# Performance work log

Measured on AMD Instinct MI355X. Metric: run time of the kernel, lower is better.

Reference implementation:

```python
import jax, jax.numpy as jnp
import numpy as np

B, S, H = 32, 2048, 1024

def setup_inputs() -> dict:
    key = jax.random.key(0)
    ks = jax.random.split(key, 8)
    sc = 1.0 / np.sqrt(H)
    return {
        "decoder_hidden": jax.random.normal(ks[0], (B, H), jnp.float32),
        "encoder_outputs": jax.random.normal(ks[1], (B, S, H), jnp.float32),
        "mask": jax.random.randint(ks[2], (B, S), 0, 2, jnp.int32),
        "Wa_w": jax.random.normal(ks[3], (H, H), jnp.float32) * sc,
        "Wa_b": jax.random.normal(ks[4], (H,), jnp.float32) * sc,
        "Ua_w": jax.random.normal(ks[5], (H, H), jnp.float32) * sc,
        "Ua_b": jax.random.normal(ks[6], (H,), jnp.float32) * sc,
        "Va_w": jax.random.normal(ks[7], (H,), jnp.float32) * sc,
        "Va_b": jnp.float32(0.0),
    }

def reference(decoder_hidden, encoder_outputs, mask, Wa_w, Wa_b, Ua_w, Ua_b, Va_w, Va_b):
    # dec proj: [B,H] -> [B,1,H]; enc proj: [B,S,H]
    dec_proj = (decoder_hidden @ Wa_w + Wa_b)[:, None, :]
    enc_proj = jnp.einsum('bsh,hk->bsk', encoder_outputs, Ua_w) + Ua_b
    energy = jnp.tanh(dec_proj + enc_proj)                      # [B,S,H]
    scores = jnp.einsum('bsh,h->bs', energy, Va_w) + Va_b       # [B,S]
    scores = jnp.where(mask == 0, jnp.float32(-1e9), scores)
    return jax.nn.softmax(scores, axis=1)
```

## Files before the change

### kernel.cpp

```cpp
#include <hip/hip_runtime.h>
#include <math.h>

#define BB 32
#define SS 2048
#define HH 1024
#define MT (BB*SS)

#define BM 256
#define BN 256
#define BK 32
#define NT (HH/BK)
#define NCH (HH/BN)
#define THREADS 512
#define BTILE 16384

typedef float  f32x4 __attribute__((ext_vector_type(4)));
typedef short  s16x8 __attribute__((ext_vector_type(8)));
typedef unsigned short u16;

__device__ inline void split1(float x, u16& h, u16& l) {
    unsigned u = __float_as_uint(x);
    h = (u16)(u >> 16);
    float hf = __uint_as_float((u >> 16) << 16);
    l = (u16)(__float_as_uint(x - hf) >> 16);
}
__device__ inline void split8v(float4 v0, float4 v1, s16x8& h, s16x8& l) {
    float x[8] = {v0.x,v0.y,v0.z,v0.w,v1.x,v1.y,v1.z,v1.w};
    #pragma unroll
    for (int j = 0; j < 8; ++j) {
        u16 hh, ll; split1(x[j], hh, ll);
        h[j] = (short)hh; l[j] = (short)ll;
    }
}

__global__ void dec_proj_kernel(const float* __restrict__ dh,
                                const float* __restrict__ Wa_w,
                                const float* __restrict__ Wa_b,
                                const float* __restrict__ Ua_b,
                                float* __restrict__ dec_proj) {
    __shared__ float sdh[HH];
    const int b   = blockIdx.x;
    const int nq  = blockIdx.y;
    const int tid = threadIdx.x;
    for (int i = tid; i < HH; i += 256) sdh[i] = dh[b*HH + i];
    __syncthreads();
    const int n = nq*256 + tid;
    float acc = Wa_b[n] + Ua_b[n];
    for (int k = 0; k < HH; ++k)
        acc = fmaf(sdh[k], Wa_w[(size_t)k*HH + n], acc);
    dec_proj[b*HH + n] = acc;
}

__global__ void transpose_convert_kernel(const float* __restrict__ Ua,
                                         u16* __restrict__ B_pre) {
    __shared__ u16 shh[64][72], shl[64][72];
    const int nb = blockIdx.x * 64, kb = blockIdx.y * 64;
    const int tid = threadIdx.x;
    const int kl = tid >> 4, nl4 = (tid & 15) * 4;
    #pragma unroll
    for (int q = 0; q < 4; ++q) {
        const int k = kl + q*16;
        float4 v = *(const float4*)&Ua[(size_t)(kb + k)*HH + nb + nl4];
        float x[4] = {v.x, v.y, v.z, v.w};
        #pragma unroll
        for (int j = 0; j < 4; ++j) {
            u16 hh, ll; split1(x[j], hh, ll);
            shh[k][nl4 + j] = hh; shl[k][nl4 + j] = ll;
        }
    }
    __syncthreads();
    const int nl = tid >> 3, kc8 = (tid & 7) * 8;
    #pragma unroll
    for (int q = 0; q < 2; ++q) {
        const int n = nb + nl + q*32;
        const int kglob = kb + kc8;
        s16x8 hv, lv;
        #pragma unroll
        for (int j = 0; j < 8; ++j) {
            hv[j] = (short)shh[kc8 + j][nl + q*32];
            lv[j] = (short)shl[kc8 + j][nl + q*32];
        }
        const int nchI = n >> 8, fI = (n >> 4) & 15, lrI = n & 15;
        const int ktI = kglob >> 5, cI = (kglob >> 3) & 3;
        const size_t base = (size_t)(nchI*32 + ktI) * BTILE;
        const size_t idxH = base + fI*512 + (cI*16 + lrI)*8;
        *(s16x8*)&B_pre[idxH]        = hv;
        *(s16x8*)&B_pre[idxH + 8192] = lv;
    }
}

__global__ __launch_bounds__(THREADS, 1)
void gemm8_kernel(const float* __restrict__ A,
                  const u16* __restrict__ B_pre,
                  const float* __restrict__ dec_proj,
                  const float* __restrict__ Va_w,
                  float* __restrict__ partials)
{
    __shared__ __align__(16) u16 AhS[2][BM*BK];
    __shared__ __align__(16) u16 AlS[2][BM*BK];
    __shared__ __align__(16) u16 BhS[2][BN*BK];
    __shared__ __align__(16) u16 BlS[2][BN*BK];

    const int bid = blockIdx.x;
    const int wg  = (bid & 7) * 128 + (bid >> 3);
    const int nch = wg & 3;
    const int mt  = wg >> 2;
    const int m0  = mt * BM, n0 = nch * BN;

    const int tid = threadIdx.x, lane = tid & 63, wid = tid >> 6;
    const int wm = wid >> 2, wn = wid & 3;
    const int lr = lane & 15, lk = lane >> 4;

    const int srow = tid >> 1, shalf = tid & 1;
    const float* Ab = A + (size_t)(m0 + srow)*HH + shalf*16;
    const int awoff0 = (srow>>4)*512 + (shalf*2    )*128 + (srow&15)*8;
    const int awoff1 = (srow>>4)*512 + (shalf*2 + 1)*128 + (srow&15)*8;
    const u16* Bt = B_pre + (size_t)nch*32*BTILE + tid*8;

    f32x4 acc[8][4];
    #pragma unroll
    for (int i = 0; i < 8; ++i)
        #pragma unroll
        for (int j = 0; j < 4; ++j) acc[i][j] = (f32x4){0.f,0.f,0.f,0.f};

    s16x8 bh[4], bl[4];
    float4 a0_, a1_, a2_, a3_;
    s16x8 bq0_, bq1_, bq2_, bq3_;

    auto loadA0  = [&](int kt) { const float* p = Ab + kt*BK;
                                 a0_ = *(const float4*)p; a1_ = *(const float4*)(p+4); };
    auto loadA1  = [&](int kt) { const float* p = Ab + kt*BK + 8;
                                 a2_ = *(const float4*)p; a3_ = *(const float4*)(p+4); };
    auto loadB01 = [&](int kt) { const u16* p = Bt + (size_t)kt*BTILE;
                                 bq0_ = *(const s16x8*)p; bq1_ = *(const s16x8*)(p+4096); };
    auto loadB23 = [&](int kt) { const u16* p = Bt + (size_t)kt*BTILE;
                                 bq2_ = *(const s16x8*)(p+8192); bq3_ = *(const s16x8*)(p+12288); };
    auto writeA0 = [&](int b) { s16x8 h,l; split8v(a0_, a1_, h, l);
                                *(s16x8*)&AhS[b][awoff0] = h; *(s16x8*)&AlS[b][awoff0] = l; };
    auto writeA1 = [&](int b) { s16x8 h,l; split8v(a2_, a3_, h, l);
                                *(s16x8*)&AhS[b][awoff1] = h; *(s16x8*)&AlS[b][awoff1] = l; };
    auto writeB  = [&](int b) { *(s16x8*)&BhS[b][tid*8]        = bq0_;
                                *(s16x8*)&BhS[b][4096 + tid*8] = bq1_;
                                *(s16x8*)&BlS[b][tid*8]        = bq2_;
                                *(s16x8*)&BlS[b][4096 + tid*8] = bq3_; };
    auto readB = [&](int cb) {
        #pragma unroll
        for (int j = 0; j < 4; ++j) {
            const int off = (wn*4 + j)*512 + lane*8;
            bh[j] = *(const s16x8*)&BhS[cb][off];
            bl[j] = *(const s16x8*)&BlS[cb][off];
        }
    };

    for (int kt = 0; kt < NT; ++kt) {
        const int  cb = kt & 1;
        const bool hn = (kt + 1 < NT);
        if (kt == 0) {
            loadA0(0); loadA1(0); loadB01(0); loadB23(0);
            writeA0(0); writeA1(0); writeB(0);
            __syncthreads();
        }
        s16x8 ah[2], al[2];
        if (hn) { loadA0(kt+1); loadB01(kt+1); }
        readB(cb);
        {   const int o0 = (wm*8 + 0)*512 + lane*8, o1 = (wm*8 + 1)*512 + lane*8;
            ah[0] = *(const s16x8*)&AhS[cb][o0]; al[0] = *(const s16x8*)&AlS[cb][o0];
            ah[1] = *(const s16x8*)&AhS[cb][o1]; al[1] = *(const s16x8*)&AlS[cb][o1]; }
        __builtin_amdgcn_s_barrier();
        __builtin_amdgcn_s_setprio(1);
        #pragma unroll
        for (int i = 0; i < 2; ++i)
            #pragma unroll
            for (int j = 0; j < 4; ++j) {
                f32x4 c = acc[i][j];
                c = __builtin_amdgcn_mfma_f32_16x16x32_bf16(ah[i], bh[j], c, 0, 0, 0);
                c = __builtin_amdgcn_mfma_f32_16x16x32_bf16(ah[i], bl[j], c, 0, 0, 0);
                c = __builtin_amdgcn_mfma_f32_16x16x32_bf16(al[i], bh[j], c, 0, 0, 0);
                acc[i][j] = c;
            }
        __builtin_amdgcn_s_setprio(0);
        __builtin_amdgcn_s_barrier();
        if (hn) { loadA1(kt+1); loadB23(kt+1); }
        {   const int o0 = (wm*8 + 2)*512 + lane*8, o1 = (wm*8 + 3)*512 + lane*8;
            ah[0] = *(const s16x8*)&AhS[cb][o0]; al[0] = *(const s16x8*)&AlS[cb][o0];
            ah[1] = *(const s16x8*)&AhS[cb][o1]; al[1] = *(const s16x8*)&AlS[cb][o1]; }
        __builtin_amdgcn_s_barrier();
        __builtin_amdgcn_s_setprio(1);
        #pragma unroll
        for (int i = 0; i < 2; ++i)
            #pragma unroll
            for (int j = 0; j < 4; ++j) {
                f32x4 c = acc[2+i][j];
                c = __builtin_amdgcn_mfma_f32_16x16x32_bf16(ah[i], bh[j], c, 0, 0, 0);
                c = __builtin_amdgcn_mfma_f32_16x16x32_bf16(ah[i], bl[j], c, 0, 0, 0);
                c = __builtin_amdgcn_mfma_f32_16x16x32_bf16(al[i], bh[j], c, 0, 0, 0);
                acc[2+i][j] = c;
            }
        __builtin_amdgcn_s_setprio(0);
        __builtin_amdgcn_s_barrier();
        if (hn) writeA0(cb ^ 1);
        {   const int o0 = (wm*8 + 4)*512 + lane*8, o1 = (wm*8 + 5)*512 + lane*8;
            ah[0] = *(const s16x8*)&AhS[cb][o0]; al[0] = *(const s16x8*)&AlS[cb][o0];
            ah[1] = *(const s16x8*)&AhS[cb][o1]; al[1] = *(const s16x8*)&AlS[cb][o1]; }
        __builtin_amdgcn_s_barrier();
        __builtin_amdgcn_s_setprio(1);
        #pragma unroll
        for (int i = 0; i < 2; ++i)
            #pragma unroll
            for (int j = 0; j < 4; ++j) {
                f32x4 c = acc[4+i][j];
                c = __builtin_amdgcn_mfma_f32_16x16x32_bf16(ah[i], bh[j], c, 0, 0, 0);
                c = __builtin_amdgcn_mfma_f32_16x16x32_bf16(ah[i], bl[j], c, 0, 0, 0);
                c = __builtin_amdgcn_mfma_f32_16x16x32_bf16(al[i], bh[j], c, 0, 0, 0);
                acc[4+i][j] = c;
            }
        __builtin_amdgcn_s_setprio(0);
        __builtin_amdgcn_s_barrier();
        if (hn) { writeA1(cb ^ 1); writeB(cb ^ 1); }
        {   const int o0 = (wm*8 + 6)*512 + lane*8, o1 = (wm*8 + 7)*512 + lane*8;
            ah[0] = *(const s16x8*)&AhS[cb][o0]; al[0] = *(const s16x8*)&AlS[cb][o0];
            ah[1] = *(const s16x8*)&AhS[cb][o1]; al[1] = *(const s16x8*)&AlS[cb][o1]; }
        __builtin_amdgcn_s_barrier();
        __builtin_amdgcn_s_setprio(1);
        #pragma unroll
        for (int i = 0; i < 2; ++i)
            #pragma unroll
            for (int j = 0; j < 4; ++j) {
                f32x4 c = acc[6+i][j];
                c = __builtin_amdgcn_mfma_f32_16x16x32_bf16(ah[i], bh[j], c, 0, 0, 0);
                c = __builtin_amdgcn_mfma_f32_16x16x32_bf16(ah[i], bl[j], c, 0, 0, 0);
                c = __builtin_amdgcn_mfma_f32_16x16x32_bf16(al[i], bh[j], c, 0, 0, 0);
                acc[6+i][j] = c;
            }
        __builtin_amdgcn_s_setprio(0);
        asm volatile("s_waitcnt vmcnt(0) lgkmcnt(0)" ::: "memory");
        __builtin_amdgcn_sched_barrier(0);
        __builtin_amdgcn_s_barrier();
    }

    const int bidx = m0 >> 11;
    float dp[4], va[4];
    #pragma unroll
    for (int j = 0; j < 4; ++j) {
        const int n = n0 + wn*64 + j*16 + lr;
        dp[j] = dec_proj[bidx*HH + n];
        va[j] = Va_w[n];
    }
    #pragma unroll
    for (int i = 0; i < 8; ++i) {
        #pragma unroll
        for (int r = 0; r < 4; ++r) {
            float s = 0.f;
            #pragma unroll
            for (int j = 0; j < 4; ++j)
                s += va[j] * tanhf(acc[i][j][r] + dp[j]);
            s += __shfl_xor(s, 1, 64);
            s += __shfl_xor(s, 2, 64);
            s += __shfl_xor(s, 4, 64);
            s += __shfl_xor(s, 8, 64);
            if (lr == 0) {
                const int m = m0 + wm*128 + i*16 + lk*4 + r;
                partials[(size_t)m*16 + nch*4 + wn] = s;
            }
        }
    }
}

__global__ void softmax_kernel(const float* __restrict__ partials,
                               const int* __restrict__ mask,
                               const float* __restrict__ vb_ptr,
                               float* __restrict__ out)
{
    const int b   = blockIdx.x;
    const int tid = threadIdx.x;
    __shared__ float sred[8];
    const float vb = vb_ptr[0];
    float sc[8];
    float mymax = -INFINITY;
    #pragma unroll
    for (int i = 0; i < 8; ++i) {
        const int s = i*256 + tid;
        const float4* p = (const float4*)&partials[((size_t)b*SS + s)*16];
        const float4 x = p[0], y = p[1], z = p[2], w = p[3];
        float v = (((x.x+x.y)+(x.z+x.w)) + ((y.x+y.y)+(y.z+y.w)))
                + (((z.x+z.y)+(z.z+z.w)) + ((w.x+w.y)+(w.z+w.w))) + vb;
        if (mask[b*SS + s] == 0) v = -1e9f;
        sc[i] = v;
        mymax = fmaxf(mymax, v);
    }
    #pragma unroll
    for (int off = 1; off < 64; off <<= 1)
        mymax = fmaxf(mymax, __shfl_xor(mymax, off, 64));
    const int wave = tid >> 6, lane = tid & 63;
    if (lane == 0) sred[wave] = mymax;
    __syncthreads();
    const float bmax = fmaxf(fmaxf(sred[0], sred[1]), fmaxf(sred[2], sred[3]));
    float ex[8], mysum = 0.f;
    #pragma unroll
    for (int i = 0; i < 8; ++i) {
        ex[i] = __expf(sc[i] - bmax);
        mysum += ex[i];
    }
    #pragma unroll
    for (int off = 1; off < 64; off <<= 1)
        mysum += __shfl_xor(mysum, off, 64);
    if (lane == 0) sred[4 + wave] = mysum;
    __syncthreads();
    const float inv = 1.f / (sred[4] + sred[5] + sred[6] + sred[7]);
    #pragma unroll
    for (int i = 0; i < 8; ++i)
        out[(size_t)b*SS + i*256 + tid] = ex[i] * inv;
}

extern "C" void kernel_launch(void* const* d_in, const int* in_sizes, int n_in,
                              void* d_out, int out_size, void* d_ws, size_t ws_size,
                              hipStream_t stream) {
    const float* dh   = (const float*)d_in[0];
    const float* enc  = (const float*)d_in[1];
    const int*   mask = (const int*)d_in[2];
    const float* Wa_w = (const float*)d_in[3];
    const float* Wa_b = (const float*)d_in[4];
    const float* Ua_w = (const float*)d_in[5];
    const float* Ua_b = (const float*)d_in[6];
    const float* Va_w = (const float*)d_in[7];
    const float* Va_b = (const float*)d_in[8];
    float* out = (float*)d_out;

    float* dec_proj = (float*)d_ws;
    float* partials = dec_proj + BB*HH;
    u16*   B_pre    = (u16*)(partials + (size_t)MT*16);

    dec_proj_kernel<<<dim3(BB, 4), 256, 0, stream>>>(dh, Wa_w, Wa_b, Ua_b, dec_proj);
    transpose_convert_kernel<<<dim3(HH/64, HH/64), 256, 0, stream>>>(Ua_w, B_pre);
    gemm8_kernel<<<(MT/BM)*NCH, THREADS, 0, stream>>>(enc, B_pre, dec_proj, Va_w, partials);
    softmax_kernel<<<BB, 256, 0, stream>>>(partials, mask, Va_b, out);
}
```

Measured before the change: 469.2 us.

## Replace LDS-staged GEMM mainloop with register-direct global loads and prefetch

The GEMM kernel drops all shared-memory staging and barriers. Each wave now loads its own A rows and pre-swizzled B fragments straight from global memory into registers, double-buffering B across k-tiles and A across fragments. This removes LDS traffic and block-wide synchronisation. In exchange there is no reuse across waves: each A row is loaded and split by 4 waves and each B fragment by 2, which raises global/L2 traffic and redundant conversion work.

```diff
diff --git a/kernel.cpp b/kernel.cpp
--- a/kernel.cpp
+++ b/kernel.cpp
@@ -90,17 +90,12 @@
 }
 
 __global__ __launch_bounds__(THREADS, 1)
-void gemm8_kernel(const float* __restrict__ A,
-                  const u16* __restrict__ B_pre,
-                  const float* __restrict__ dec_proj,
-                  const float* __restrict__ Va_w,
-                  float* __restrict__ partials)
+void gemm_reg_kernel(const float* __restrict__ A,
+                     const u16* __restrict__ B_pre,
+                     const float* __restrict__ dec_proj,
+                     const float* __restrict__ Va_w,
+                     float* __restrict__ partials)
 {
-    __shared__ __align__(16) u16 AhS[2][BM*BK];
-    __shared__ __align__(16) u16 AlS[2][BM*BK];
-    __shared__ __align__(16) u16 BhS[2][BN*BK];
-    __shared__ __align__(16) u16 BlS[2][BN*BK];
-
     const int bid = blockIdx.x;
     const int wg  = (bid & 7) * 128 + (bid >> 3);
     const int nch = wg & 3;
@@ -111,11 +106,8 @@
     const int wm = wid >> 2, wn = wid & 3;
     const int lr = lane & 15, lk = lane >> 4;
 
-    const int srow = tid >> 1, shalf = tid & 1;
-    const float* Ab = A + (size_t)(m0 + srow)*HH + shalf*16;
-    const int awoff0 = (srow>>4)*512 + (shalf*2    )*128 + (srow&15)*8;
-    const int awoff1 = (srow>>4)*512 + (shalf*2 + 1)*128 + (srow&15)*8;
-    const u16* Bt = B_pre + (size_t)nch*32*BTILE + tid*8;
+    const u16*   Bt = B_pre + (size_t)nch*NT*BTILE + (wn*4)*512 + lane*8;
+    const float* Aw = A + (size_t)(m0 + wm*128 + lr)*HH + lk*8;
 
     f32x4 acc[8][4];
     #pragma unroll
@@ -123,119 +115,50 @@
         #pragma unroll
         for (int j = 0; j < 4; ++j) acc[i][j] = (f32x4){0.f,0.f,0.f,0.f};
 
-    s16x8 bh[4], bl[4];
-    float4 a0_, a1_, a2_, a3_;
-    s16x8 bq0_, bq1_, bq2_, bq3_;
-
-    auto loadA0  = [&](int kt) { const float* p = Ab + kt*BK;
-                                 a0_ = *(const float4*)p; a1_ = *(const float4*)(p+4); };
-    auto loadA1  = [&](int kt) { const float* p = Ab + kt*BK + 8;
-                                 a2_ = *(const float4*)p; a3_ = *(const float4*)(p+4); };
-    auto loadB01 = [&](int kt) { const u16* p = Bt + (size_t)kt*BTILE;
-                                 bq0_ = *(const s16x8*)p; bq1_ = *(const s16x8*)(p+4096); };
-    auto loadB23 = [&](int kt) { const u16* p = Bt + (size_t)kt*BTILE;
-                                 bq2_ = *(const s16x8*)(p+8192); bq3_ = *(const s16x8*)(p+12288); };
-    auto writeA0 = [&](int b) { s16x8 h,l; split8v(a0_, a1_, h, l);
-                                *(s16x8*)&AhS[b][awoff0] = h; *(s16x8*)&AlS[b][awoff0] = l; };
-    auto writeA1 = [&](int b) { s16x8 h,l; split8v(a2_, a3_, h, l);
-                                *(s16x8*)&AhS[b][awoff1] = h; *(s16x8*)&AlS[b][awoff1] = l; };
-    auto writeB  = [&](int b) { *(s16x8*)&BhS[b][tid*8]        = bq0_;
-                                *(s16x8*)&BhS[b][4096 + tid*8] = bq1_;
-                                *(s16x8*)&BlS[b][tid*8]        = bq2_;
-                                *(s16x8*)&BlS[b][4096 + tid*8] = bq3_; };
-    auto readB = [&](int cb) {
+    s16x8 bhA[4], blA[4], bhB[4], blB[4];
+    float4 ar0[2], ar1[2];
+
+    auto loadB = [&](int kt, s16x8 (&bh)[4], s16x8 (&bl)[4]) {
+        const u16* p = Bt + (size_t)kt*BTILE;
         #pragma unroll
         for (int j = 0; j < 4; ++j) {
-            const int off = (wn*4 + j)*512 + lane*8;
-            bh[j] = *(const s16x8*)&BhS[cb][off];
-            bl[j] = *(const s16x8*)&BlS[cb][off];
+            bh[j] = *(const s16x8*)(p + j*512);
+            bl[j] = *(const s16x8*)(p + 8192 + j*512);
         }
     };
-
-    for (int kt = 0; kt < NT; ++kt) {
-        const int  cb = kt & 1;
-        const bool hn = (kt + 1 < NT);
-        if (kt == 0) {
-            loadA0(0); loadA1(0); loadB01(0); loadB23(0);
-            writeA0(0); writeA1(0); writeB(0);
-            __syncthreads();
-        }
-        s16x8 ah[2], al[2];
-        if (hn) { loadA0(kt+1); loadB01(kt+1); }
-        readB(cb);
-        {   const int o0 = (wm*8 + 0)*512 + lane*8, o1 = (wm*8 + 1)*512 + lane*8;
-            ah[0] = *(const s16x8*)&AhS[cb][o0]; al[0] = *(const s16x8*)&AlS[cb][o0];
-            ah[1] = *(const s16x8*)&AhS[cb][o1]; al[1] = *(const s16x8*)&AlS[cb][o1]; }
-        __builtin_amdgcn_s_barrier();
-        __builtin_amdgcn_s_setprio(1);
-        #pragma unroll
-        for (int i = 0; i < 2; ++i)
+    auto loadA = [&](int kt, int f, float4& r0, float4& r1) {
+        const float* p = Aw + (size_t)f*16*HH + kt*BK;
+        r0 = *(const float4*)p;
+        r1 = *(const float4*)(p + 4);
+    };
+
+    auto tile = [&](int kt, s16x8 (&bch)[4], s16x8 (&bcl)[4],
+                            s16x8 (&bnh)[4], s16x8 (&bnl)[4]) {
+        const int ktn = (kt + 1 < NT) ? kt + 1 : kt;
+        #pragma unroll
+        for (int f = 0; f < 8; ++f) {
+            if (f == 0) loadB(ktn, bnh, bnl);
+            if (f < 7) loadA(kt,  f + 1, ar0[(f+1)&1], ar1[(f+1)&1]);
+            else       loadA(ktn, 0,     ar0[0],       ar1[0]);
+            s16x8 ah, al;
+            split8v(ar0[f&1], ar1[f&1], ah, al);
             #pragma unroll
             for (int j = 0; j < 4; ++j) {
-                f32x4 c = acc[i][j];
-                c = __builtin_amdgcn_mfma_f32_16x16x32_bf16(ah[i], bh[j], c, 0, 0, 0);
-                c = __builtin_amdgcn_mfma_f32_16x16x32_bf16(ah[i], bl[j], c, 0, 0, 0);
-                c = __builtin_amdgcn_mfma_f32_16x16x32_bf16(al[i], bh[j], c, 0, 0, 0);
-                acc[i][j] = c;
+                f32x4 c = acc[f][j];
+                c = __builtin_amdgcn_mfma_f32_16x16x32_bf16(ah, bch[j], c, 0, 0, 0);
+                c = __builtin_amdgcn_mfma_f32_16x16x32_bf16(ah, bcl[j], c, 0, 0, 0);
+                c = __builtin_amdgcn_mfma_f32_16x16x32_bf16(al, bch[j], c, 0, 0, 0);
+                acc[f][j] = c;
             }
-        __builtin_amdgcn_s_setprio(0);
-        __builtin_amdgcn_s_barrier();
-        if (hn) { loadA1(kt+1); loadB23(kt+1); }
-        {   const int o0 = (wm*8 + 2)*512 + lane*8, o1 = (wm*8 + 3)*512 + lane*8;
-            ah[0] = *(const s16x8*)&AhS[cb][o0]; al[0] = *(const s16x8*)&AlS[cb][o0];
-            ah[1] = *(const s16x8*)&AhS[cb][o1]; al[1] = *(const s16x8*)&AlS[cb][o1]; }
-        __builtin_amdgcn_s_barrier();
-        __builtin_amdgcn_s_setprio(1);
-        #pragma unroll
-        for (int i = 0; i < 2; ++i)
-            #pragma unroll
-            for (int j = 0; j < 4; ++j) {
-                f32x4 c = acc[2+i][j];
-                c = __builtin_amdgcn_mfma_f32_16x16x32_bf16(ah[i], bh[j], c, 0, 0, 0);
-                c = __builtin_amdgcn_mfma_f32_16x16x32_bf16(ah[i], bl[j], c, 0, 0, 0);
-                c = __builtin_amdgcn_mfma_f32_16x16x32_bf16(al[i], bh[j], c, 0, 0, 0);
-                acc[2+i][j] = c;
-            }
-        __builtin_amdgcn_s_setprio(0);
-        __builtin_amdgcn_s_barrier();
-        if (hn) writeA0(cb ^ 1);
-        {   const int o0 = (wm*8 + 4)*512 + lane*8, o1 = (wm*8 + 5)*512 + lane*8;
-            ah[0] = *(const s16x8*)&AhS[cb][o0]; al[0] = *(const s16x8*)&AlS[cb][o0];
-            ah[1] = *(const s16x8*)&AhS[cb][o1]; al[1] = *(const s16x8*)&AlS[cb][o1]; }
-        __builtin_amdgcn_s_barrier();
-        __builtin_amdgcn_s_setprio(1);
-        #pragma unroll
-        for (int i = 0; i < 2; ++i)
-            #pragma unroll
-            for (int j = 0; j < 4; ++j) {
-                f32x4 c = acc[4+i][j];
-                c = __builtin_amdgcn_mfma_f32_16x16x32_bf16(ah[i], bh[j], c, 0, 0, 0);
-                c = __builtin_amdgcn_mfma_f32_16x16x32_bf16(ah[i], bl[j], c, 0, 0, 0);
-                c = __builtin_amdgcn_mfma_f32_16x16x32_bf16(al[i], bh[j], c, 0, 0, 0);
-                acc[4+i][j] = c;
-            }
-        __builtin_amdgcn_s_setprio(0);
-        __builtin_amdgcn_s_barrier();
-        if (hn) { writeA1(cb ^ 1); writeB(cb ^ 1); }
-        {   const int o0 = (wm*8 + 6)*512 + lane*8, o1 = (wm*8 + 7)*512 + lane*8;
-            ah[0] = *(const s16x8*)&AhS[cb][o0]; al[0] = *(const s16x8*)&AlS[cb][o0];
-            ah[1] = *(const s16x8*)&AhS[cb][o1]; al[1] = *(const s16x8*)&AlS[cb][o1]; }
-        __builtin_amdgcn_s_barrier();
-        __builtin_amdgcn_s_setprio(1);
-        #pragma unroll
-        for (int i = 0; i < 2; ++i)
-            #pragma unroll
-            for (int j = 0; j < 4; ++j) {
-                f32x4 c = acc[6+i][j];
-                c = __builtin_amdgcn_mfma_f32_16x16x32_bf16(ah[i], bh[j], c, 0, 0, 0);
-                c = __builtin_amdgcn_mfma_f32_16x16x32_bf16(ah[i], bl[j], c, 0, 0, 0);
-                c = __builtin_amdgcn_mfma_f32_16x16x32_bf16(al[i], bh[j], c, 0, 0, 0);
-                acc[6+i][j] = c;
-            }
-        __builtin_amdgcn_s_setprio(0);
-        asm volatile("s_waitcnt vmcnt(0) lgkmcnt(0)" ::: "memory");
-        __builtin_amdgcn_sched_barrier(0);
-        __builtin_amdgcn_s_barrier();
+        }
+    };
+
+    loadB(0, bhA, blA);
+    loadA(0, 0, ar0[0], ar1[0]);
+
+    for (int kt2 = 0; kt2 < NT; kt2 += 2) {
+        tile(kt2,     bhA, blA, bhB, blB);
+        tile(kt2 + 1, bhB, blB, bhA, blA);
     }
 
     const int bidx = m0 >> 11;
@@ -332,6 +255,6 @@
 
     dec_proj_kernel<<<dim3(BB, 4), 256, 0, stream>>>(dh, Wa_w, Wa_b, Ua_b, dec_proj);
     transpose_convert_kernel<<<dim3(HH/64, HH/64), 256, 0, stream>>>(Ua_w, B_pre);
-    gemm8_kernel<<<(MT/BM)*NCH, THREADS, 0, stream>>>(enc, B_pre, dec_proj, Va_w, partials);
+    gemm_reg_kernel<<<(MT/BM)*NCH, THREADS, 0, stream>>>(enc, B_pre, dec_proj, Va_w, partials);
     softmax_kernel<<<BB, 256, 0, stream>>>(partials, mask, Va_b, out);
 }
```

New measurement: 779.2 us. 66.1% more time.
